# Kernel tuning notes

Hardware: AMD Instinct MI355X
Metric: run time of the kernel (lower is better)

## Reference

```python
import jax, jax.numpy as jnp
import numpy as np

N, E, D, K = 60000, 1200000, 64, 3

def setup_inputs() -> dict:
    key = jax.random.key(0)
    k1, k2, k3 = jax.random.split(key, 3)
    feat = jax.random.normal(k1, (N, D), dtype=jnp.float32)
    src = jax.random.randint(k2, (E,), 0, N)
    dst = jax.random.randint(k3, (E,), 0, N)
    lambda_max = jnp.ones((1,), dtype=jnp.float32)
    return {"feat": feat, "src": src, "dst": dst, "lambda_max": lambda_max}

def reference(feat, src, dst, lambda_max):
    n = feat.shape[0]
    # in-degree of each node = number of edges whose dst is that node
    deg = jax.ops.segment_sum(jnp.ones(src.shape[0], dtype=feat.dtype), dst, num_segments=n)
    d_invsqrt = jnp.maximum(deg, 1.0) ** -0.5  # [N]
    d_invsqrt = d_invsqrt[:, None]             # [N,1]
    re_norm = 2.0 / lambda_max                 # [1], broadcasts over nodes/feats

    def unn_laplacian(x):
        # x * D^-1/2 A D^-1/2 via gather over src, scatter-sum to dst
        return d_invsqrt * jax.ops.segment_sum((x * d_invsqrt)[src], dst, num_segments=n)

    X0 = feat
    outs = [X0]
    if K > 1:
        h = unn_laplacian(X0)
        X1 = -re_norm * h + X0 * (re_norm - 1.0)
        outs.append(X1)
    for _ in range(2, K):
        h = unn_laplacian(X1)
        Xi = -2.0 * re_norm * h + X1 * 2.0 * (re_norm - 1.0) - X0
        outs.append(Xi)
        X1, X0 = Xi, X1
    Xt = jnp.concatenate(outs, axis=1)  # [N, K*D]
    return jax.nn.relu(Xt)
```

## Files before the change

kernel.cpp:

```cpp
#include <hip/hip_runtime.h>


#define DF 64
#define NBK 512
#define BCAP 2976
#define EPT 32

__device__ __forceinline__ unsigned bf16rne(float f) {
    unsigned u = __float_as_uint(f);
    return (u + 0x7FFFu + ((u >> 16) & 1u)) >> 16;
}
__device__ __forceinline__ float bflo(unsigned u) { return __uint_as_float(u << 16); }
__device__ __forceinline__ float bfhi(unsigned u) { return __uint_as_float(u & 0xFFFF0000u); }

__global__ __launch_bounds__(256) void partition_kernel(
    const int* __restrict__ src, const int* __restrict__ dst,
    int* __restrict__ bcursor, int* __restrict__ staged, int E) {
    __shared__ int hist[NBK];
    __shared__ int cur[NBK];
    int tid = threadIdx.x;
    for (int i = tid; i < NBK; i += 256) hist[i] = 0;
    __syncthreads();
    int e0 = blockIdx.x * (256 * EPT);
    #pragma unroll
    for (int k = 0; k < EPT / 4; k++) {
        int e = e0 + (k * 256 + tid) * 4;
        if (e + 3 < E) {
            int4 d4 = *(const int4*)(dst + e);
            atomicAdd(&hist[d4.x >> 7], 1);
            atomicAdd(&hist[d4.y >> 7], 1);
            atomicAdd(&hist[d4.z >> 7], 1);
            atomicAdd(&hist[d4.w >> 7], 1);
        } else {
            for (int j = 0; j < 4; j++) {
                int e1 = e + j;
                if (e1 < E) atomicAdd(&hist[dst[e1] >> 7], 1);
            }
        }
    }
    __syncthreads();
    for (int i = tid; i < NBK; i += 256) {
        int h = hist[i];
        cur[i] = h ? atomicAdd(&bcursor[i], h) : 0;
    }
    __syncthreads();
    #pragma unroll
    for (int k = 0; k < EPT / 4; k++) {
        int e = e0 + (k * 256 + tid) * 4;
        if (e + 3 < E) {
            int4 s4 = *(const int4*)(src + e);
            int4 d4 = *(const int4*)(dst + e);
            int ss[4] = {s4.x, s4.y, s4.z, s4.w};
            int dd[4] = {d4.x, d4.y, d4.z, d4.w};
            #pragma unroll
            for (int j = 0; j < 4; j++) {
                int b = dd[j] >> 7;
                int pos = atomicAdd(&cur[b], 1);
                if (pos < BCAP) staged[b * BCAP + pos] = (ss[j] << 7) | (dd[j] & 127);
            }
        } else {
            for (int j = 0; j < 4; j++) {
                int e1 = e + j;
                if (e1 < E) {
                    int s = src[e1], d = dst[e1];
                    int b = d >> 7;
                    int pos = atomicAdd(&cur[b], 1);
                    if (pos < BCAP) staged[b * BCAP + pos] = (s << 7) | (d & 127);
                }
            }
        }
    }
}

__global__ __launch_bounds__(256) void bucket_csr_kernel(
    const int* __restrict__ staged, const int* __restrict__ bcursor,
    const float* __restrict__ feat,
    unsigned short* __restrict__ col, int2* __restrict__ begend,
    float* __restrict__ dinv, uint2* __restrict__ featb,
    float* __restrict__ out, int n) {
    __shared__ int sin[BCAP];
    __shared__ int sout[BCAP];
    __shared__ int hist[128];
    __shared__ int scn[128];
    __shared__ int cur[128];
    __shared__ float sdinv[128];
    int tid = threadIdx.x;
    int b = blockIdx.x;
    int cnt = bcursor[b]; if (cnt > BCAP) cnt = BCAP;
    if (tid < 128) hist[tid] = 0;
    __syncthreads();
    const int* sb = staged + b * BCAP;
    for (int i = tid; i < cnt; i += 256) {
        int e = sb[i];
        sin[i] = e;
        atomicAdd(&hist[e & 127], 1);
    }
    __syncthreads();
    int v = 0;
    if (tid < 128) { v = hist[tid]; scn[tid] = v; }
    __syncthreads();
    for (int off = 1; off < 128; off <<= 1) {
        int x = 0, y = 0;
        if (tid < 128) { x = scn[tid]; y = (tid >= off) ? scn[tid - off] : 0; }
        __syncthreads();
        if (tid < 128) scn[tid] = x + y;
        __syncthreads();
    }
    int excl = 0;
    if (tid < 128) { excl = scn[tid] - v; cur[tid] = excl; }
    __syncthreads();
    for (int i = tid; i < cnt; i += 256) {
        int e = sin[i];
        int pos = atomicAdd(&cur[e & 127], 1);
        sout[pos] = e >> 7;
    }
    __syncthreads();
    unsigned* cbu = (unsigned*)(col + (size_t)b * BCAP);
    int cnt2 = (cnt + 1) >> 1;
    for (int i = tid; i < cnt2; i += 256) {
        int lo = sout[2 * i];
        int hi = (2 * i + 1 < cnt) ? sout[2 * i + 1] : 0;
        cbu[i] = (unsigned)lo | ((unsigned)hi << 16);
    }
    int base_node = b << 7;
    int rows = n - base_node; if (rows > 128) rows = 128;
    if (tid < 128) {
        float dv = 1.0f;
        int node = base_node + tid;
        if (tid < rows) {
            int d = hist[tid];
            begend[node] = make_int2(b * BCAP + excl, b * BCAP + excl + d);
            if (d < 1) d = 1;
            dv = rsqrtf((float)d);
            dinv[node] = dv;
        }
        sdinv[tid] = dv;
    }
    __syncthreads();
    for (int idx = tid; idx < rows * 16; idx += 256) {
        int nl = idx >> 4, subl = idx & 15;
        int node = base_node + nl;
        float w = sdinv[nl];
        float4 a = *(const float4*)(feat + (size_t)node * DF + subl * 4);
        uint2 pk;
        pk.x = bf16rne(a.x * w) | (bf16rne(a.y * w) << 16);
        pk.y = bf16rne(a.z * w) | (bf16rne(a.w * w) << 16);
        featb[(size_t)node * 16 + subl] = pk;
        float4 r0 = make_float4(fmaxf(a.x, 0.f), fmaxf(a.y, 0.f),
                                fmaxf(a.z, 0.f), fmaxf(a.w, 0.f));
        *(float4*)(out + (size_t)node * (3 * DF) + subl * 4) = r0;
    }
}

__global__ __launch_bounds__(256) void prop1_kernel(
    const float* __restrict__ feat, const uint4* __restrict__ featb4,
    const int2* __restrict__ begend, const unsigned short* __restrict__ col,
    const float* __restrict__ dinv, const float* __restrict__ lambda_max,
    uint4* __restrict__ x1n4, float* __restrict__ out, int n) {
    int node = (int)((blockIdx.x * blockDim.x + threadIdx.x) >> 6);
    if (node >= n) return;
    int lane = threadIdx.x & 63;
    int grp = lane >> 3;
    int sub = lane & 7;
    int2 be = begend[node];
    int beg = be.x, end = be.y;
    float dn = dinv[node];
    float rn = 2.0f / lambda_max[0];
    float a0 = 0.f, a1 = 0.f, a2 = 0.f, a3 = 0.f;
    float a4 = 0.f, a5 = 0.f, a6 = 0.f, a7 = 0.f;
    int i = beg + grp;
    for (; i + 8 < end; i += 16) {
        int s0 = col[i], s1 = col[i + 8];
        uint4 v0 = featb4[(size_t)s0 * 8 + sub];
        uint4 v1 = featb4[(size_t)s1 * 8 + sub];
        a0 += bflo(v0.x) + bflo(v1.x); a1 += bfhi(v0.x) + bfhi(v1.x);
        a2 += bflo(v0.y) + bflo(v1.y); a3 += bfhi(v0.y) + bfhi(v1.y);
        a4 += bflo(v0.z) + bflo(v1.z); a5 += bfhi(v0.z) + bfhi(v1.z);
        a6 += bflo(v0.w) + bflo(v1.w); a7 += bfhi(v0.w) + bfhi(v1.w);
    }
    if (i < end) {
        int s0 = col[i];
        uint4 v0 = featb4[(size_t)s0 * 8 + sub];
        a0 += bflo(v0.x); a1 += bfhi(v0.x);
        a2 += bflo(v0.y); a3 += bfhi(v0.y);
        a4 += bflo(v0.z); a5 += bfhi(v0.z);
        a6 += bflo(v0.w); a7 += bfhi(v0.w);
    }
    a0 += __shfl_xor(a0, 8); a0 += __shfl_xor(a0, 16); a0 += __shfl_xor(a0, 32);
    a1 += __shfl_xor(a1, 8); a1 += __shfl_xor(a1, 16); a1 += __shfl_xor(a1, 32);
    a2 += __shfl_xor(a2, 8); a2 += __shfl_xor(a2, 16); a2 += __shfl_xor(a2, 32);
    a3 += __shfl_xor(a3, 8); a3 += __shfl_xor(a3, 16); a3 += __shfl_xor(a3, 32);
    a4 += __shfl_xor(a4, 8); a4 += __shfl_xor(a4, 16); a4 += __shfl_xor(a4, 32);
    a5 += __shfl_xor(a5, 8); a5 += __shfl_xor(a5, 16); a5 += __shfl_xor(a5, 32);
    a6 += __shfl_xor(a6, 8); a6 += __shfl_xor(a6, 16); a6 += __shfl_xor(a6, 32);
    a7 += __shfl_xor(a7, 8); a7 += __shfl_xor(a7, 16); a7 += __shfl_xor(a7, 32);
    if (grp == 0) {
        const float* fb = feat + (size_t)node * DF + sub * 8;
        float4 xa = *(const float4*)fb;
        float4 xb = *(const float4*)(fb + 4);
        float c1 = rn - 1.0f;
        float dnrn = rn * dn;
        float x10 = c1 * xa.x - dnrn * a0, x11 = c1 * xa.y - dnrn * a1;
        float x12 = c1 * xa.z - dnrn * a2, x13 = c1 * xa.w - dnrn * a3;
        float x14 = c1 * xb.x - dnrn * a4, x15 = c1 * xb.y - dnrn * a5;
        float x16 = c1 * xb.z - dnrn * a6, x17 = c1 * xb.w - dnrn * a7;
        uint4 p;
        p.x = bf16rne(x10 * dn) | (bf16rne(x11 * dn) << 16);
        p.y = bf16rne(x12 * dn) | (bf16rne(x13 * dn) << 16);
        p.z = bf16rne(x14 * dn) | (bf16rne(x15 * dn) << 16);
        p.w = bf16rne(x16 * dn) | (bf16rne(x17 * dn) << 16);
        x1n4[(size_t)node * 8 + sub] = p;
        float* ob = out + (size_t)node * (3 * DF) + DF + sub * 8;
        *(float4*)ob = make_float4(fmaxf(x10, 0.f), fmaxf(x11, 0.f),
                                   fmaxf(x12, 0.f), fmaxf(x13, 0.f));
        *(float4*)(ob + 4) = make_float4(fmaxf(x14, 0.f), fmaxf(x15, 0.f),
                                         fmaxf(x16, 0.f), fmaxf(x17, 0.f));
    }
}

__global__ __launch_bounds__(256) void prop2_kernel(
    const float* __restrict__ feat, const uint4* __restrict__ x1n4,
    const int2* __restrict__ begend, const unsigned short* __restrict__ col,
    const float* __restrict__ dinv, const float* __restrict__ lambda_max,
    float* __restrict__ out, int n) {
    int node = (int)((blockIdx.x * blockDim.x + threadIdx.x) >> 6);
    if (node >= n) return;
    int lane = threadIdx.x & 63;
    int grp = lane >> 3;
    int sub = lane & 7;
    int2 be = begend[node];
    int beg = be.x, end = be.y;
    float dn = dinv[node];
    float rn = 2.0f / lambda_max[0];
    float a0 = 0.f, a1 = 0.f, a2 = 0.f, a3 = 0.f;
    float a4 = 0.f, a5 = 0.f, a6 = 0.f, a7 = 0.f;
    int i = beg + grp;
    for (; i + 8 < end; i += 16) {
        int s0 = col[i], s1 = col[i + 8];
        uint4 v0 = x1n4[(size_t)s0 * 8 + sub];
        uint4 v1 = x1n4[(size_t)s1 * 8 + sub];
        a0 += bflo(v0.x) + bflo(v1.x); a1 += bfhi(v0.x) + bfhi(v1.x);
        a2 += bflo(v0.y) + bflo(v1.y); a3 += bfhi(v0.y) + bfhi(v1.y);
        a4 += bflo(v0.z) + bflo(v1.z); a5 += bfhi(v0.z) + bfhi(v1.z);
        a6 += bflo(v0.w) + bflo(v1.w); a7 += bfhi(v0.w) + bfhi(v1.w);
    }
    if (i < end) {
        int s0 = col[i];
        uint4 v0 = x1n4[(size_t)s0 * 8 + sub];
        a0 += bflo(v0.x); a1 += bfhi(v0.x);
        a2 += bflo(v0.y); a3 += bfhi(v0.y);
        a4 += bflo(v0.z); a5 += bfhi(v0.z);
        a6 += bflo(v0.w); a7 += bfhi(v0.w);
    }
    a0 += __shfl_xor(a0, 8); a0 += __shfl_xor(a0, 16); a0 += __shfl_xor(a0, 32);
    a1 += __shfl_xor(a1, 8); a1 += __shfl_xor(a1, 16); a1 += __shfl_xor(a1, 32);
    a2 += __shfl_xor(a2, 8); a2 += __shfl_xor(a2, 16); a2 += __shfl_xor(a2, 32);
    a3 += __shfl_xor(a3, 8); a3 += __shfl_xor(a3, 16); a3 += __shfl_xor(a3, 32);
    a4 += __shfl_xor(a4, 8); a4 += __shfl_xor(a4, 16); a4 += __shfl_xor(a4, 32);
    a5 += __shfl_xor(a5, 8); a5 += __shfl_xor(a5, 16); a5 += __shfl_xor(a5, 32);
    a6 += __shfl_xor(a6, 8); a6 += __shfl_xor(a6, 16); a6 += __shfl_xor(a6, 32);
    a7 += __shfl_xor(a7, 8); a7 += __shfl_xor(a7, 16); a7 += __shfl_xor(a7, 32);
    if (grp == 0) {
        const float* fb = feat + (size_t)node * DF + sub * 8;
        float4 xa = *(const float4*)fb;
        float4 xb = *(const float4*)(fb + 4);
        uint4 xo = x1n4[(size_t)node * 8 + sub];
        float inv_dn = 1.0f / dn;
        float c2 = 2.0f * (rn - 1.0f);
        float s2c = 2.0f * rn * dn;
        float x20 = c2 * (bflo(xo.x) * inv_dn) - s2c * a0 - xa.x;
        float x21 = c2 * (bfhi(xo.x) * inv_dn) - s2c * a1 - xa.y;
        float x22 = c2 * (bflo(xo.y) * inv_dn) - s2c * a2 - xa.z;
        float x23 = c2 * (bfhi(xo.y) * inv_dn) - s2c * a3 - xa.w;
        float x24 = c2 * (bflo(xo.z) * inv_dn) - s2c * a4 - xb.x;
        float x25 = c2 * (bfhi(xo.z) * inv_dn) - s2c * a5 - xb.y;
        float x26 = c2 * (bflo(xo.w) * inv_dn) - s2c * a6 - xb.z;
        float x27 = c2 * (bfhi(xo.w) * inv_dn) - s2c * a7 - xb.w;
        float* ob = out + (size_t)node * (3 * DF) + 2 * DF + sub * 8;
        *(float4*)ob = make_float4(fmaxf(x20, 0.f), fmaxf(x21, 0.f),
                                   fmaxf(x22, 0.f), fmaxf(x23, 0.f));
        *(float4*)(ob + 4) = make_float4(fmaxf(x24, 0.f), fmaxf(x25, 0.f),
                                         fmaxf(x26, 0.f), fmaxf(x27, 0.f));
    }
}

extern "C" void kernel_launch(void* const* d_in, const int* in_sizes, int n_in,
                              void* d_out, int out_size, void* d_ws, size_t ws_size,
                              hipStream_t stream) {
    const float* feat = (const float*)d_in[0];
    const int* src = (const int*)d_in[1];
    const int* dst = (const int*)d_in[2];
    const float* lambda_max = (const float*)d_in[3];
    const int n = in_sizes[0] / DF;
    const int E = in_sizes[1];
    float* out = (float*)d_out;

    const int nbk = (n + 127) >> 7;

    auto align256 = [](size_t x) { return (x + 255) & ~(size_t)255; };
    char* ws = (char*)d_ws;
    int* bcursor = (int*)ws;   ws += align256(NBK * sizeof(int));
    float* dinv = (float*)ws;  ws += align256((size_t)n * sizeof(float));
    int2* begend = (int2*)ws;  ws += align256((size_t)n * sizeof(int2));
    unsigned short* col = (unsigned short*)ws;
    ws += align256((size_t)nbk * BCAP * sizeof(unsigned short));
    int* staged = (int*)ws;    ws += align256((size_t)nbk * BCAP * sizeof(int));
    uint2* featb = (uint2*)ws; ws += align256((size_t)n * DF * 2);
    uint4* x1n = (uint4*)ws;

    hipMemsetAsync(bcursor, 0, NBK * sizeof(int), stream);
    partition_kernel<<<(E + 256 * EPT - 1) / (256 * EPT), 256, 0, stream>>>(
        src, dst, bcursor, staged, E);
    bucket_csr_kernel<<<nbk, 256, 0, stream>>>(staged, bcursor, feat, col,
                                               begend, dinv, featb, out, n);
    prop1_kernel<<<(n + 3) / 4, 256, 0, stream>>>(feat, (const uint4*)featb,
                                                  begend, col, dinv, lambda_max,
                                                  x1n, out, n);
    prop2_kernel<<<(n + 3) / 4, 256, 0, stream>>>(feat, x1n, begend, col,
                                                  dinv, lambda_max, out, n);
}
```

Measured before the change: 169.1 us.

## Split bf16 feature tables into half-planes and propagate each half separately

```diff
diff --git a/kernel.cpp b/kernel.cpp
--- a/kernel.cpp
+++ b/kernel.cpp
@@ -4,7 +4,11 @@
 #define DF 64
 #define NBK 512
 #define BCAP 2976
-#define EPT 32
+#define EPT 8
+
+typedef float f32x4 __attribute__((ext_vector_type(4)));
+typedef unsigned u32x4 __attribute__((ext_vector_type(4)));
+typedef unsigned u32x2 __attribute__((ext_vector_type(2)));
 
 __device__ __forceinline__ unsigned bf16rne(float f) {
     unsigned u = __float_as_uint(f);
@@ -137,150 +141,131 @@
         sdinv[tid] = dv;
     }
     __syncthreads();
+    size_t plane_u2 = (size_t)n * 8;
     for (int idx = tid; idx < rows * 16; idx += 256) {
         int nl = idx >> 4, subl = idx & 15;
         int node = base_node + nl;
         float w = sdinv[nl];
-        float4 a = *(const float4*)(feat + (size_t)node * DF + subl * 4);
-        uint2 pk;
-        pk.x = bf16rne(a.x * w) | (bf16rne(a.y * w) << 16);
-        pk.y = bf16rne(a.z * w) | (bf16rne(a.w * w) << 16);
-        featb[(size_t)node * 16 + subl] = pk;
-        float4 r0 = make_float4(fmaxf(a.x, 0.f), fmaxf(a.y, 0.f),
-                                fmaxf(a.z, 0.f), fmaxf(a.w, 0.f));
-        *(float4*)(out + (size_t)node * (3 * DF) + subl * 4) = r0;
+        f32x4 a = __builtin_nontemporal_load(
+            (const f32x4*)(feat + (size_t)node * DF + subl * 4));
+        u32x2 pk = { bf16rne(a[0] * w) | (bf16rne(a[1] * w) << 16),
+                     bf16rne(a[2] * w) | (bf16rne(a[3] * w) << 16) };
+        __builtin_nontemporal_store(pk,
+            (u32x2*)(featb + (size_t)(subl >> 3) * plane_u2
+                     + (size_t)node * 8 + (subl & 7)));
+        f32x4 r0 = { fmaxf(a[0], 0.f), fmaxf(a[1], 0.f),
+                     fmaxf(a[2], 0.f), fmaxf(a[3], 0.f) };
+        __builtin_nontemporal_store(r0,
+            (f32x4*)(out + (size_t)node * (3 * DF) + subl * 4));
     }
 }
 
 __global__ __launch_bounds__(256) void prop1_kernel(
-    const float* __restrict__ feat, const uint4* __restrict__ featb4,
+    const float* __restrict__ feat, const uint4* __restrict__ fbp,
     const int2* __restrict__ begend, const unsigned short* __restrict__ col,
     const float* __restrict__ dinv, const float* __restrict__ lambda_max,
-    uint4* __restrict__ x1n4, float* __restrict__ out, int n) {
+    uint4* __restrict__ x1p, float* __restrict__ out, int n, int half) {
     int node = (int)((blockIdx.x * blockDim.x + threadIdx.x) >> 6);
     if (node >= n) return;
     int lane = threadIdx.x & 63;
-    int grp = lane >> 3;
-    int sub = lane & 7;
+    int grp = lane >> 2;
+    int sub = lane & 3;
     int2 be = begend[node];
-    int beg = be.x, end = be.y;
     float dn = dinv[node];
     float rn = 2.0f / lambda_max[0];
     float a0 = 0.f, a1 = 0.f, a2 = 0.f, a3 = 0.f;
     float a4 = 0.f, a5 = 0.f, a6 = 0.f, a7 = 0.f;
-    int i = beg + grp;
-    for (; i + 8 < end; i += 16) {
-        int s0 = col[i], s1 = col[i + 8];
-        uint4 v0 = featb4[(size_t)s0 * 8 + sub];
-        uint4 v1 = featb4[(size_t)s1 * 8 + sub];
-        a0 += bflo(v0.x) + bflo(v1.x); a1 += bfhi(v0.x) + bfhi(v1.x);
-        a2 += bflo(v0.y) + bflo(v1.y); a3 += bfhi(v0.y) + bfhi(v1.y);
-        a4 += bflo(v0.z) + bflo(v1.z); a5 += bfhi(v0.z) + bfhi(v1.z);
-        a6 += bflo(v0.w) + bflo(v1.w); a7 += bfhi(v0.w) + bfhi(v1.w);
-    }
-    if (i < end) {
+    for (int i = be.x + grp; i < be.y; i += 16) {
         int s0 = col[i];
-        uint4 v0 = featb4[(size_t)s0 * 8 + sub];
+        uint4 v0 = fbp[(size_t)s0 * 4 + sub];
         a0 += bflo(v0.x); a1 += bfhi(v0.x);
         a2 += bflo(v0.y); a3 += bfhi(v0.y);
         a4 += bflo(v0.z); a5 += bfhi(v0.z);
         a6 += bflo(v0.w); a7 += bfhi(v0.w);
     }
-    a0 += __shfl_xor(a0, 8); a0 += __shfl_xor(a0, 16); a0 += __shfl_xor(a0, 32);
-    a1 += __shfl_xor(a1, 8); a1 += __shfl_xor(a1, 16); a1 += __shfl_xor(a1, 32);
-    a2 += __shfl_xor(a2, 8); a2 += __shfl_xor(a2, 16); a2 += __shfl_xor(a2, 32);
-    a3 += __shfl_xor(a3, 8); a3 += __shfl_xor(a3, 16); a3 += __shfl_xor(a3, 32);
-    a4 += __shfl_xor(a4, 8); a4 += __shfl_xor(a4, 16); a4 += __shfl_xor(a4, 32);
-    a5 += __shfl_xor(a5, 8); a5 += __shfl_xor(a5, 16); a5 += __shfl_xor(a5, 32);
-    a6 += __shfl_xor(a6, 8); a6 += __shfl_xor(a6, 16); a6 += __shfl_xor(a6, 32);
-    a7 += __shfl_xor(a7, 8); a7 += __shfl_xor(a7, 16); a7 += __shfl_xor(a7, 32);
+    a0 += __shfl_xor(a0, 4); a0 += __shfl_xor(a0, 8); a0 += __shfl_xor(a0, 16); a0 += __shfl_xor(a0, 32);
+    a1 += __shfl_xor(a1, 4); a1 += __shfl_xor(a1, 8); a1 += __shfl_xor(a1, 16); a1 += __shfl_xor(a1, 32);
+    a2 += __shfl_xor(a2, 4); a2 += __shfl_xor(a2, 8); a2 += __shfl_xor(a2, 16); a2 += __shfl_xor(a2, 32);
+    a3 += __shfl_xor(a3, 4); a3 += __shfl_xor(a3, 8); a3 += __shfl_xor(a3, 16); a3 += __shfl_xor(a3, 32);
+    a4 += __shfl_xor(a4, 4); a4 += __shfl_xor(a4, 8); a4 += __shfl_xor(a4, 16); a4 += __shfl_xor(a4, 32);
+    a5 += __shfl_xor(a5, 4); a5 += __shfl_xor(a5, 8); a5 += __shfl_xor(a5, 16); a5 += __shfl_xor(a5, 32);
+    a6 += __shfl_xor(a6, 4); a6 += __shfl_xor(a6, 8); a6 += __shfl_xor(a6, 16); a6 += __shfl_xor(a6, 32);
+    a7 += __shfl_xor(a7, 4); a7 += __shfl_xor(a7, 8); a7 += __shfl_xor(a7, 16); a7 += __shfl_xor(a7, 32);
     if (grp == 0) {
-        const float* fb = feat + (size_t)node * DF + sub * 8;
-        float4 xa = *(const float4*)fb;
-        float4 xb = *(const float4*)(fb + 4);
+        const float* fb = feat + (size_t)node * DF + half * 32 + sub * 8;
+        f32x4 xa = __builtin_nontemporal_load((const f32x4*)fb);
+        f32x4 xb = __builtin_nontemporal_load((const f32x4*)(fb + 4));
         float c1 = rn - 1.0f;
         float dnrn = rn * dn;
-        float x10 = c1 * xa.x - dnrn * a0, x11 = c1 * xa.y - dnrn * a1;
-        float x12 = c1 * xa.z - dnrn * a2, x13 = c1 * xa.w - dnrn * a3;
-        float x14 = c1 * xb.x - dnrn * a4, x15 = c1 * xb.y - dnrn * a5;
-        float x16 = c1 * xb.z - dnrn * a6, x17 = c1 * xb.w - dnrn * a7;
-        uint4 p;
-        p.x = bf16rne(x10 * dn) | (bf16rne(x11 * dn) << 16);
-        p.y = bf16rne(x12 * dn) | (bf16rne(x13 * dn) << 16);
-        p.z = bf16rne(x14 * dn) | (bf16rne(x15 * dn) << 16);
-        p.w = bf16rne(x16 * dn) | (bf16rne(x17 * dn) << 16);
-        x1n4[(size_t)node * 8 + sub] = p;
-        float* ob = out + (size_t)node * (3 * DF) + DF + sub * 8;
-        *(float4*)ob = make_float4(fmaxf(x10, 0.f), fmaxf(x11, 0.f),
-                                   fmaxf(x12, 0.f), fmaxf(x13, 0.f));
-        *(float4*)(ob + 4) = make_float4(fmaxf(x14, 0.f), fmaxf(x15, 0.f),
-                                         fmaxf(x16, 0.f), fmaxf(x17, 0.f));
+        float x10 = c1 * xa[0] - dnrn * a0, x11 = c1 * xa[1] - dnrn * a1;
+        float x12 = c1 * xa[2] - dnrn * a2, x13 = c1 * xa[3] - dnrn * a3;
+        float x14 = c1 * xb[0] - dnrn * a4, x15 = c1 * xb[1] - dnrn * a5;
+        float x16 = c1 * xb[2] - dnrn * a6, x17 = c1 * xb[3] - dnrn * a7;
+        u32x4 p = { bf16rne(x10 * dn) | (bf16rne(x11 * dn) << 16),
+                    bf16rne(x12 * dn) | (bf16rne(x13 * dn) << 16),
+                    bf16rne(x14 * dn) | (bf16rne(x15 * dn) << 16),
+                    bf16rne(x16 * dn) | (bf16rne(x17 * dn) << 16) };
+        __builtin_nontemporal_store(p, (u32x4*)(x1p + (size_t)node * 4 + sub));
+        float* ob = out + (size_t)node * (3 * DF) + DF + half * 32 + sub * 8;
+        f32x4 r0 = { fmaxf(x10, 0.f), fmaxf(x11, 0.f), fmaxf(x12, 0.f), fmaxf(x13, 0.f) };
+        f32x4 r1 = { fmaxf(x14, 0.f), fmaxf(x15, 0.f), fmaxf(x16, 0.f), fmaxf(x17, 0.f) };
+        __builtin_nontemporal_store(r0, (f32x4*)ob);
+        __builtin_nontemporal_store(r1, (f32x4*)(ob + 4));
     }
 }
 
 __global__ __launch_bounds__(256) void prop2_kernel(
-    const float* __restrict__ feat, const uint4* __restrict__ x1n4,
+    const float* __restrict__ feat, const uint4* __restrict__ x1p,
     const int2* __restrict__ begend, const unsigned short* __restrict__ col,
     const float* __restrict__ dinv, const float* __restrict__ lambda_max,
-    float* __restrict__ out, int n) {
+    float* __restrict__ out, int n, int half) {
     int node = (int)((blockIdx.x * blockDim.x + threadIdx.x) >> 6);
     if (node >= n) return;
     int lane = threadIdx.x & 63;
-    int grp = lane >> 3;
-    int sub = lane & 7;
+    int grp = lane >> 2;
+    int sub = lane & 3;
     int2 be = begend[node];
-    int beg = be.x, end = be.y;
     float dn = dinv[node];
     float rn = 2.0f / lambda_max[0];
     float a0 = 0.f, a1 = 0.f, a2 = 0.f, a3 = 0.f;
     float a4 = 0.f, a5 = 0.f, a6 = 0.f, a7 = 0.f;
-    int i = beg + grp;
-    for (; i + 8 < end; i += 16) {
-        int s0 = col[i], s1 = col[i + 8];
-        uint4 v0 = x1n4[(size_t)s0 * 8 + sub];
-        uint4 v1 = x1n4[(size_t)s1 * 8 + sub];
-        a0 += bflo(v0.x) + bflo(v1.x); a1 += bfhi(v0.x) + bfhi(v1.x);
-        a2 += bflo(v0.y) + bflo(v1.y); a3 += bfhi(v0.y) + bfhi(v1.y);
-        a4 += bflo(v0.z) + bflo(v1.z); a5 += bfhi(v0.z) + bfhi(v1.z);
-        a6 += bflo(v0.w) + bflo(v1.w); a7 += bfhi(v0.w) + bfhi(v1.w);
-    }
-    if (i < end) {
+    for (int i = be.x + grp; i < be.y; i += 16) {
         int s0 = col[i];
-        uint4 v0 = x1n4[(size_t)s0 * 8 + sub];
+        uint4 v0 = x1p[(size_t)s0 * 4 + sub];
         a0 += bflo(v0.x); a1 += bfhi(v0.x);
         a2 += bflo(v0.y); a3 += bfhi(v0.y);
         a4 += bflo(v0.z); a5 += bfhi(v0.z);
         a6 += bflo(v0.w); a7 += bfhi(v0.w);
     }
-    a0 += __shfl_xor(a0, 8); a0 += __shfl_xor(a0, 16); a0 += __shfl_xor(a0, 32);
-    a1 += __shfl_xor(a1, 8); a1 += __shfl_xor(a1, 16); a1 += __shfl_xor(a1, 32);
-    a2 += __shfl_xor(a2, 8); a2 += __shfl_xor(a2, 16); a2 += __shfl_xor(a2, 32);
-    a3 += __shfl_xor(a3, 8); a3 += __shfl_xor(a3, 16); a3 += __shfl_xor(a3, 32);
-    a4 += __shfl_xor(a4, 8); a4 += __shfl_xor(a4, 16); a4 += __shfl_xor(a4, 32);
-    a5 += __shfl_xor(a5, 8); a5 += __shfl_xor(a5, 16); a5 += __shfl_xor(a5, 32);
-    a6 += __shfl_xor(a6, 8); a6 += __shfl_xor(a6, 16); a6 += __shfl_xor(a6, 32);
-    a7 += __shfl_xor(a7, 8); a7 += __shfl_xor(a7, 16); a7 += __shfl_xor(a7, 32);
+    a0 += __shfl_xor(a0, 4); a0 += __shfl_xor(a0, 8); a0 += __shfl_xor(a0, 16); a0 += __shfl_xor(a0, 32);
+    a1 += __shfl_xor(a1, 4); a1 += __shfl_xor(a1, 8); a1 += __shfl_xor(a1, 16); a1 += __shfl_xor(a1, 32);
+    a2 += __shfl_xor(a2, 4); a2 += __shfl_xor(a2, 8); a2 += __shfl_xor(a2, 16); a2 += __shfl_xor(a2, 32);
+    a3 += __shfl_xor(a3, 4); a3 += __shfl_xor(a3, 8); a3 += __shfl_xor(a3, 16); a3 += __shfl_xor(a3, 32);
+    a4 += __shfl_xor(a4, 4); a4 += __shfl_xor(a4, 8); a4 += __shfl_xor(a4, 16); a4 += __shfl_xor(a4, 32);
+    a5 += __shfl_xor(a5, 4); a5 += __shfl_xor(a5, 8); a5 += __shfl_xor(a5, 16); a5 += __shfl_xor(a5, 32);
+    a6 += __shfl_xor(a6, 4); a6 += __shfl_xor(a6, 8); a6 += __shfl_xor(a6, 16); a6 += __shfl_xor(a6, 32);
+    a7 += __shfl_xor(a7, 4); a7 += __shfl_xor(a7, 8); a7 += __shfl_xor(a7, 16); a7 += __shfl_xor(a7, 32);
     if (grp == 0) {
-        const float* fb = feat + (size_t)node * DF + sub * 8;
-        float4 xa = *(const float4*)fb;
-        float4 xb = *(const float4*)(fb + 4);
-        uint4 xo = x1n4[(size_t)node * 8 + sub];
+        const float* fb = feat + (size_t)node * DF + half * 32 + sub * 8;
+        f32x4 xa = __builtin_nontemporal_load((const f32x4*)fb);
+        f32x4 xb = __builtin_nontemporal_load((const f32x4*)(fb + 4));
+        uint4 xo = x1p[(size_t)node * 4 + sub];
         float inv_dn = 1.0f / dn;
         float c2 = 2.0f * (rn - 1.0f);
         float s2c = 2.0f * rn * dn;
-        float x20 = c2 * (bflo(xo.x) * inv_dn) - s2c * a0 - xa.x;
-        float x21 = c2 * (bfhi(xo.x) * inv_dn) - s2c * a1 - xa.y;
-        float x22 = c2 * (bflo(xo.y) * inv_dn) - s2c * a2 - xa.z;
-        float x23 = c2 * (bfhi(xo.y) * inv_dn) - s2c * a3 - xa.w;
-        float x24 = c2 * (bflo(xo.z) * inv_dn) - s2c * a4 - xb.x;
-        float x25 = c2 * (bfhi(xo.z) * inv_dn) - s2c * a5 - xb.y;
-        float x26 = c2 * (bflo(xo.w) * inv_dn) - s2c * a6 - xb.z;
-        float x27 = c2 * (bfhi(xo.w) * inv_dn) - s2c * a7 - xb.w;
-        float* ob = out + (size_t)node * (3 * DF) + 2 * DF + sub * 8;
-        *(float4*)ob = make_float4(fmaxf(x20, 0.f), fmaxf(x21, 0.f),
-                                   fmaxf(x22, 0.f), fmaxf(x23, 0.f));
-        *(float4*)(ob + 4) = make_float4(fmaxf(x24, 0.f), fmaxf(x25, 0.f),
-                                         fmaxf(x26, 0.f), fmaxf(x27, 0.f));
+        float x20 = c2 * (bflo(xo.x) * inv_dn) - s2c * a0 - xa[0];
+        float x21 = c2 * (bfhi(xo.x) * inv_dn) - s2c * a1 - xa[1];
+        float x22 = c2 * (bflo(xo.y) * inv_dn) - s2c * a2 - xa[2];
+        float x23 = c2 * (bfhi(xo.y) * inv_dn) - s2c * a3 - xa[3];
+        float x24 = c2 * (bflo(xo.z) * inv_dn) - s2c * a4 - xb[0];
+        float x25 = c2 * (bfhi(xo.z) * inv_dn) - s2c * a5 - xb[1];
+        float x26 = c2 * (bflo(xo.w) * inv_dn) - s2c * a6 - xb[2];
+        float x27 = c2 * (bfhi(xo.w) * inv_dn) - s2c * a7 - xb[3];
+        float* ob = out + (size_t)node * (3 * DF) + 2 * DF + half * 32 + sub * 8;
+        f32x4 r0 = { fmaxf(x20, 0.f), fmaxf(x21, 0.f), fmaxf(x22, 0.f), fmaxf(x23, 0.f) };
+        f32x4 r1 = { fmaxf(x24, 0.f), fmaxf(x25, 0.f), fmaxf(x26, 0.f), fmaxf(x27, 0.f) };
+        __builtin_nontemporal_store(r0, (f32x4*)ob);
+        __builtin_nontemporal_store(r1, (f32x4*)(ob + 4));
     }
 }
 
@@ -308,14 +293,20 @@
     uint2* featb = (uint2*)ws; ws += align256((size_t)n * DF * 2);
     uint4* x1n = (uint4*)ws;
 
+    const size_t plane4 = (size_t)n * 4;
+
     hipMemsetAsync(bcursor, 0, NBK * sizeof(int), stream);
     partition_kernel<<<(E + 256 * EPT - 1) / (256 * EPT), 256, 0, stream>>>(
         src, dst, bcursor, staged, E);
     bucket_csr_kernel<<<nbk, 256, 0, stream>>>(staged, bcursor, feat, col,
                                                begend, dinv, featb, out, n);
-    prop1_kernel<<<(n + 3) / 4, 256, 0, stream>>>(feat, (const uint4*)featb,
-                                                  begend, col, dinv, lambda_max,
-                                                  x1n, out, n);
+    const uint4* fb4 = (const uint4*)featb;
+    prop1_kernel<<<(n + 3) / 4, 256, 0, stream>>>(feat, fb4, begend, col,
+                                                  dinv, lambda_max, x1n, out, n, 0);
+    prop1_kernel<<<(n + 3) / 4, 256, 0, stream>>>(feat, fb4 + plane4, begend, col,
+                                                  dinv, lambda_max, x1n + plane4, out, n, 1);
     prop2_kernel<<<(n + 3) / 4, 256, 0, stream>>>(feat, x1n, begend, col,
-                                                  dinv, lambda_max, out, n);
-}
+                                                  dinv, lambda_max, out, n, 0);
+    prop2_kernel<<<(n + 3) / 4, 256, 0, stream>>>(feat, x1n + plane4, begend, col,
+                                                  dinv, lambda_max, out, n, 1);
+}
```

New measurement: 241.4 us. 1.43x slower.
